# Optimization experiments

Measured on AMD Instinct MI355X. Metric: run time of the kernel, lower is better.

Reference implementation:

```python
import jax, jax.numpy as jnp
import numpy as np

N_NODES = 100000
N_EDGES = 1600000
N_GRAPHS = 256
IN_DIM, HID, OUT_DIM = 20, 128, 30954


def setup_inputs() -> dict:
    key = jax.random.key(0)
    ks = jax.random.split(key, 9)
    x = jax.random.normal(ks[0], (N_NODES, IN_DIM), dtype=jnp.float32)
    edge_index = jax.random.randint(ks[1], (2, N_EDGES), 0, N_NODES, dtype=jnp.int64)
    batch = jnp.sort(jax.random.randint(ks[2], (N_NODES,), 0, N_GRAPHS, dtype=jnp.int64))
    s = 0.05
    W1 = jax.random.normal(ks[3], (IN_DIM, HID), dtype=jnp.float32) * s
    b1 = jax.random.normal(ks[4], (HID,), dtype=jnp.float32) * s
    W2 = jax.random.normal(ks[5], (HID, HID), dtype=jnp.float32) * s
    b2 = jax.random.normal(ks[6], (HID,), dtype=jnp.float32) * s
    Wc = jax.random.normal(ks[7], (HID, OUT_DIM), dtype=jnp.float32) * s
    bc = jax.random.normal(ks[8], (OUT_DIM,), dtype=jnp.float32) * s
    return {"x": x, "edge_index": edge_index, "batch": batch,
            "W1": W1, "b1": b1, "W2": W2, "b2": b2, "Wc": Wc, "bc": bc}


def _gcn_norm(edge_index, n_nodes):
    # add self loops (PyG GCNConv default), symmetric normalization
    loops = jnp.arange(n_nodes, dtype=edge_index.dtype)
    src = jnp.concatenate([edge_index[0], loops])
    dst = jnp.concatenate([edge_index[1], loops])
    deg = jax.ops.segment_sum(jnp.ones_like(dst, dtype=jnp.float32), dst,
                              num_segments=n_nodes)
    dinv = jnp.where(deg > 0, jax.lax.rsqrt(deg), 0.0)
    norm = dinv[src] * dinv[dst]  # [E+N]
    return src, dst, norm


def _gcn_conv(x, src, dst, norm, W, b, n_nodes):
    h = x @ W                              # [N, out] transform first (fewer msg flops)
    msg = h[src] * norm[:, None]           # gather + scale
    out = jax.ops.segment_sum(msg, dst, num_segments=n_nodes)
    return out + b


def reference(x, edge_index, batch, W1, b1, W2, b2, Wc, bc):
    n = x.shape[0]
    src, dst, norm = _gcn_norm(edge_index, n)
    h = jax.nn.relu(_gcn_conv(x, src, dst, norm, W1, b1, n))
    # dropout is identity in eval mode
    h = jax.nn.relu(_gcn_conv(h, src, dst, norm, W2, b2, n))
    # global mean pool per graph
    sums = jax.ops.segment_sum(h, batch, num_segments=N_GRAPHS)       # [G, HID]
    cnts = jax.ops.segment_sum(jnp.ones((n,), jnp.float32), batch,
                               num_segments=N_GRAPHS)
    pooled = sums / jnp.maximum(cnts, 1.0)[:, None]
    return pooled @ Wc + bc  # [G, OUT_DIM]
```

## Files before the change

### kernel.cpp

```cpp
#include <hip/hip_runtime.h>

#define HID 128
#define SCAN_B 256

__device__ __forceinline__ float bf_lo(unsigned int u) { return __uint_as_float(u << 16); }
__device__ __forceinline__ float bf_hi(unsigned int u) { return __uint_as_float(u & 0xFFFF0000u); }
__device__ __forceinline__ unsigned short f2bf(float f) {
    unsigned int u = __float_as_uint(f);
    unsigned int r = (u + 0x7FFFu + ((u >> 16) & 1u)) >> 16;
    return (unsigned short)r;
}

__global__ void detect_kernel(const unsigned int* __restrict__ p, int* __restrict__ flag) {
    if (threadIdx.x == 0 && blockIdx.x == 0) {
        int is64 = 1;
        for (int i = 0; i < 64; ++i) {
            if (p[2 * i + 1] != 0u) { is64 = 0; break; }
        }
        *flag = is64;
    }
}

__global__ void cvtdeg_kernel(const void* __restrict__ p, int* __restrict__ out,
                              int* __restrict__ deg, int E, const int* __restrict__ flag) {
    int i = blockIdx.x * blockDim.x + threadIdx.x;
    if (i < 2 * E) {
        int v = (*flag) ? (int)((const long long*)p)[i] : ((const int*)p)[i];
        out[i] = v;
        if (i >= E) atomicAdd(&deg[v], 1);
    }
}

__global__ void zero_kernel(float4* __restrict__ p, long long n4) {
    long long i = (long long)blockIdx.x * blockDim.x + threadIdx.x;
    long long stride = (long long)gridDim.x * blockDim.x;
    for (; i < n4; i += stride) p[i] = make_float4(0.f, 0.f, 0.f, 0.f);
}

__global__ void cvtx_kernel(const float* __restrict__ x, unsigned short* __restrict__ xb, int n) {
    int i = blockIdx.x * blockDim.x + threadIdx.x;
    if (i < n) xb[i] = f2bf(x[i]);
}

__global__ __launch_bounds__(SCAN_B) void scan1_kernel(const int* __restrict__ deg,
                                                       int* __restrict__ incl,
                                                       int* __restrict__ blockSums, int N) {
    __shared__ int s[SCAN_B];
    int i = blockIdx.x * SCAN_B + threadIdx.x;
    int v = (i < N) ? deg[i] : 0;
    s[threadIdx.x] = v;
    __syncthreads();
#pragma unroll
    for (int off = 1; off < SCAN_B; off <<= 1) {
        int t = (threadIdx.x >= off) ? s[threadIdx.x - off] : 0;
        __syncthreads();
        s[threadIdx.x] += t;
        __syncthreads();
    }
    if (i < N) incl[i] = s[threadIdx.x];
    if (threadIdx.x == SCAN_B - 1) blockSums[blockIdx.x] = s[SCAN_B - 1];
}

__global__ __launch_bounds__(1024) void scan2_kernel(int* __restrict__ blockSums, int nb) {
    __shared__ int s[1024];
    int v = (threadIdx.x < nb) ? blockSums[threadIdx.x] : 0;
    s[threadIdx.x] = v;
    __syncthreads();
#pragma unroll
    for (int off = 1; off < 1024; off <<= 1) {
        int t = (threadIdx.x >= off) ? s[threadIdx.x - off] : 0;
        __syncthreads();
        s[threadIdx.x] += t;
        __syncthreads();
    }
    if (threadIdx.x < nb) blockSums[threadIdx.x] = (threadIdx.x > 0) ? s[threadIdx.x - 1] : 0;
}

__global__ void scan3_kernel(const int* __restrict__ incl, const int* __restrict__ deg,
                             const int* __restrict__ blockSums, int* __restrict__ rowstart,
                             float* __restrict__ dinv, int* __restrict__ cursor,
                             int N, int E) {
    int i = blockIdx.x * blockDim.x + threadIdx.x;
    if (i < N) {
        int d = deg[i];
        rowstart[i] = incl[i] - d + blockSums[i / SCAN_B];
        dinv[i] = rsqrtf((float)(d + 1));
        cursor[i] = 0;
    }
    if (i == 0) rowstart[N] = E;
}

__global__ void scatter_kernel(const int* __restrict__ src, const int* __restrict__ dst,
                               const int* __restrict__ rowstart, int* __restrict__ cursor,
                               int2* __restrict__ elist, const float* __restrict__ dinv, int E) {
    int e = blockIdx.x * blockDim.x + threadIdx.x;
    if (e >= E) return;
    int s = src[e], d = dst[e];
    int pos = rowstart[d] + atomicAdd(&cursor[d], 1);
    float nm = dinv[s] * dinv[d];
    elist[pos] = make_int2(s, __float_as_int(nm));
}

__global__ void gstart_kernel(const void* __restrict__ bt, const int* __restrict__ flag,
                              int* __restrict__ gstart, int N, int G) {
    int g = blockIdx.x * blockDim.x + threadIdx.x;
    if (g > G) return;
    int is64 = *flag;
    int lo = 0, hi = N;
    while (lo < hi) {
        int mid = (lo + hi) >> 1;
        int v = is64 ? (int)((const long long*)bt)[mid] : ((const int*)bt)[mid];
        if (v < g) lo = mid + 1; else hi = mid;
    }
    gstart[g] = lo;
}

__global__ __launch_bounds__(256) void agg_lin1_kernel(const float* __restrict__ x,
                                                       const unsigned int* __restrict__ xb32,
                                                       const float* __restrict__ W,
                                                       const float* __restrict__ b,
                                                       unsigned int* __restrict__ h1b,
                                                       const int* __restrict__ rowstart,
                                                       const int2* __restrict__ elist,
                                                       const float* __restrict__ dinv,
                                                       int N, int IN) {
    __shared__ float Ws[20 * HID];
    __shared__ float zs[8][20];
    const int tid = threadIdx.x;
    for (int i = tid; i < IN * HID; i += 256) Ws[i] = W[i];

    const int g      = tid >> 5;
    const int lane32 = tid & 31;
    const int slot   = lane32 >> 4;
    const int l      = lane32 & 15;
    const int node   = blockIdx.x * 8 + g;
    const int half   = IN >> 1;
    const bool act   = (node < N) && (l < half);

    float accx = 0.f, accy = 0.f;
    if (node < N) {
        int beg = rowstart[node], end = rowstart[node + 1];
        int e = beg + slot;
        for (; e + 6 < end; e += 8) {
            int2 p0 = elist[e];
            int2 p1 = elist[e + 2];
            int2 p2 = elist[e + 4];
            int2 p3 = elist[e + 6];
            unsigned int u0 = act ? xb32[(size_t)p0.x * half + l] : 0u;
            unsigned int u1 = act ? xb32[(size_t)p1.x * half + l] : 0u;
            unsigned int u2 = act ? xb32[(size_t)p2.x * half + l] : 0u;
            unsigned int u3 = act ? xb32[(size_t)p3.x * half + l] : 0u;
            float n0 = __int_as_float(p0.y), n1 = __int_as_float(p1.y);
            float n2 = __int_as_float(p2.y), n3 = __int_as_float(p3.y);
            accx += bf_lo(u0) * n0 + bf_lo(u1) * n1 + bf_lo(u2) * n2 + bf_lo(u3) * n3;
            accy += bf_hi(u0) * n0 + bf_hi(u1) * n1 + bf_hi(u2) * n2 + bf_hi(u3) * n3;
        }
        for (; e < end; e += 2) {
            int2 p0 = elist[e];
            unsigned int u0 = act ? xb32[(size_t)p0.x * half + l] : 0u;
            float n0 = __int_as_float(p0.y);
            accx += bf_lo(u0) * n0;
            accy += bf_hi(u0) * n0;
        }
    }
    accx += __shfl_xor(accx, 16, 64);
    accy += __shfl_xor(accy, 16, 64);
    if (node < N && slot == 0 && l < half) {
        float di = dinv[node];
        float dd = di * di;
        zs[g][2 * l]     = accx + x[(size_t)node * IN + 2 * l] * dd;
        zs[g][2 * l + 1] = accy + x[(size_t)node * IN + 2 * l + 1] * dd;
    }
    __syncthreads();

    if (node < N) {
        const int j = lane32;
        float4 acc4 = ((const float4*)b)[j];
        for (int k = 0; k < IN; ++k) {
            float zv = zs[g][k];
            float4 w = *(const float4*)&Ws[k * HID + j * 4];
            acc4.x += zv * w.x; acc4.y += zv * w.y;
            acc4.z += zv * w.z; acc4.w += zv * w.w;
        }
        acc4.x = fmaxf(acc4.x, 0.f); acc4.y = fmaxf(acc4.y, 0.f);
        acc4.z = fmaxf(acc4.z, 0.f); acc4.w = fmaxf(acc4.w, 0.f);
        uint2 st;
        st.x = (unsigned)f2bf(acc4.x) | ((unsigned)f2bf(acc4.y) << 16);
        st.y = (unsigned)f2bf(acc4.z) | ((unsigned)f2bf(acc4.w) << 16);
        ((uint2*)h1b)[(size_t)node * 32 + j] = st;
    }
}

#define TBM 64
#define TBN 64
#define TBK 32
#define XLD (TBM + 4)

__global__ __launch_bounds__(256) void gemm128_kernel(const unsigned int* __restrict__ Ab,
                                                      const float* __restrict__ W,
                                                      unsigned short* __restrict__ Cb, int N) {
    __shared__ float xs[TBK][XLD];
    __shared__ float wsh[TBK][TBN + 4];
    const int tid = threadIdx.x;
    const int n0 = blockIdx.x * TBM;
    const int c0 = blockIdx.y * TBN;
    const int ng = tid >> 4;
    const int cg = tid & 15;
    const int anode = tid >> 2;
    const int af    = tid & 3;
    const int wk    = tid >> 4;
    const int wc    = tid & 15;

    const uint4* Av = (const uint4*)Ab;

    float acc[4][4] = {};

    for (int k0 = 0; k0 < HID; k0 += TBK) {
        {
            int gn = n0 + anode;
            uint4 u = make_uint4(0u, 0u, 0u, 0u);
            if (gn < N) u = Av[(size_t)gn * 16 + (k0 >> 3) + af];
            int kb = af * 8;
            xs[kb + 0][anode] = bf_lo(u.x);
            xs[kb + 1][anode] = bf_hi(u.x);
            xs[kb + 2][anode] = bf_lo(u.y);
            xs[kb + 3][anode] = bf_hi(u.y);
            xs[kb + 4][anode] = bf_lo(u.z);
            xs[kb + 5][anode] = bf_hi(u.z);
            xs[kb + 6][anode] = bf_lo(u.w);
            xs[kb + 7][anode] = bf_hi(u.w);
        }
#pragma unroll
        for (int r = 0; r < 2; ++r) {
            int kk = wk + r * 16;
            *(float4*)&wsh[kk][wc * 4] =
                *(const float4*)(W + (size_t)(k0 + kk) * HID + c0 + wc * 4);
        }
        __syncthreads();
#pragma unroll
        for (int kk = 0; kk < TBK; ++kk) {
            float a[4], b[4];
            *(float4*)a = *(const float4*)&xs[kk][ng * 4];
            *(float4*)b = *(const float4*)&wsh[kk][cg * 4];
#pragma unroll
            for (int m = 0; m < 4; ++m)
#pragma unroll
                for (int n = 0; n < 4; ++n) acc[m][n] += a[m] * b[n];
        }
        __syncthreads();
    }

#pragma unroll
    for (int m = 0; m < 4; ++m) {
        int gn = n0 + ng * 4 + m;
        if (gn < N) {
            ushort4 st;
            st.x = f2bf(acc[m][0]); st.y = f2bf(acc[m][1]);
            st.z = f2bf(acc[m][2]); st.w = f2bf(acc[m][3]);
            *(ushort4*)(Cb + (size_t)gn * HID + c0 + cg * 4) = st;
        }
    }
}

__global__ __launch_bounds__(256) void csr_aggb_kernel(const unsigned short* __restrict__ h2b,
                                                       unsigned short* __restrict__ outb,
                                                       const int* __restrict__ rowstart,
                                                       const int2* __restrict__ elist,
                                                       const float* __restrict__ dinv,
                                                       const float* __restrict__ bias,
                                                       int N) {
    int node = blockIdx.x * 16 + (threadIdx.x >> 4);
    if (node >= N) return;
    int q = threadIdx.x & 15;
    const uint4* hv = (const uint4*)h2b;
    float acc[8] = {};
    int beg = rowstart[node], end = rowstart[node + 1];
    int e = beg;
    for (; e + 3 < end; e += 4) {
        int2 p0 = elist[e];
        int2 p1 = elist[e + 1];
        int2 p2 = elist[e + 2];
        int2 p3 = elist[e + 3];
        uint4 a0 = hv[(size_t)p0.x * 16 + q];
        uint4 a1 = hv[(size_t)p1.x * 16 + q];
        uint4 a2 = hv[(size_t)p2.x * 16 + q];
        uint4 a3 = hv[(size_t)p3.x * 16 + q];
        float n0 = __int_as_float(p0.y), n1 = __int_as_float(p1.y);
        float n2 = __int_as_float(p2.y), n3 = __int_as_float(p3.y);
        acc[0] += bf_lo(a0.x) * n0 + bf_lo(a1.x) * n1 + bf_lo(a2.x) * n2 + bf_lo(a3.x) * n3;
        acc[1] += bf_hi(a0.x) * n0 + bf_hi(a1.x) * n1 + bf_hi(a2.x) * n2 + bf_hi(a3.x) * n3;
        acc[2] += bf_lo(a0.y) * n0 + bf_lo(a1.y) * n1 + bf_lo(a2.y) * n2 + bf_lo(a3.y) * n3;
        acc[3] += bf_hi(a0.y) * n0 + bf_hi(a1.y) * n1 + bf_hi(a2.y) * n2 + bf_hi(a3.y) * n3;
        acc[4] += bf_lo(a0.z) * n0 + bf_lo(a1.z) * n1 + bf_lo(a2.z) * n2 + bf_lo(a3.z) * n3;
        acc[5] += bf_hi(a0.z) * n0 + bf_hi(a1.z) * n1 + bf_hi(a2.z) * n2 + bf_hi(a3.z) * n3;
        acc[6] += bf_lo(a0.w) * n0 + bf_lo(a1.w) * n1 + bf_lo(a2.w) * n2 + bf_lo(a3.w) * n3;
        acc[7] += bf_hi(a0.w) * n0 + bf_hi(a1.w) * n1 + bf_hi(a2.w) * n2 + bf_hi(a3.w) * n3;
    }
    for (; e < end; ++e) {
        int2 p0 = elist[e];
        uint4 a0 = hv[(size_t)p0.x * 16 + q];
        float n0 = __int_as_float(p0.y);
        acc[0] += bf_lo(a0.x) * n0; acc[1] += bf_hi(a0.x) * n0;
        acc[2] += bf_lo(a0.y) * n0; acc[3] += bf_hi(a0.y) * n0;
        acc[4] += bf_lo(a0.z) * n0; acc[5] += bf_hi(a0.z) * n0;
        acc[6] += bf_lo(a0.w) * n0; acc[7] += bf_hi(a0.w) * n0;
    }
    float di = dinv[node];
    float dd = di * di;
    uint4 sv = hv[(size_t)node * 16 + q];
    float self[8] = { bf_lo(sv.x), bf_hi(sv.x), bf_lo(sv.y), bf_hi(sv.y),
                      bf_lo(sv.z), bf_hi(sv.z), bf_lo(sv.w), bf_hi(sv.w) };
    float4 b0 = ((const float4*)bias)[2 * q];
    float4 b1 = ((const float4*)bias)[2 * q + 1];
    float r[8];
    r[0] = fmaxf(acc[0] + self[0] * dd + b0.x, 0.f);
    r[1] = fmaxf(acc[1] + self[1] * dd + b0.y, 0.f);
    r[2] = fmaxf(acc[2] + self[2] * dd + b0.z, 0.f);
    r[3] = fmaxf(acc[3] + self[3] * dd + b0.w, 0.f);
    r[4] = fmaxf(acc[4] + self[4] * dd + b1.x, 0.f);
    r[5] = fmaxf(acc[5] + self[5] * dd + b1.y, 0.f);
    r[6] = fmaxf(acc[6] + self[6] * dd + b1.z, 0.f);
    r[7] = fmaxf(acc[7] + self[7] * dd + b1.w, 0.f);
    uint4 st;
    st.x = (unsigned)f2bf(r[0]) | ((unsigned)f2bf(r[1]) << 16);
    st.y = (unsigned)f2bf(r[2]) | ((unsigned)f2bf(r[3]) << 16);
    st.z = (unsigned)f2bf(r[4]) | ((unsigned)f2bf(r[5]) << 16);
    st.w = (unsigned)f2bf(r[6]) | ((unsigned)f2bf(r[7]) << 16);
    ((uint4*)outb)[(size_t)node * 16 + q] = st;
}

__global__ __launch_bounds__(1024) void pool2_kernel(const unsigned short* __restrict__ hb,
                                                     const int* __restrict__ gstart,
                                                     float* __restrict__ meanp, int G) {
    int g = blockIdx.x;
    int part = threadIdx.x >> 7;
    int j = threadIdx.x & 127;
    int beg = gstart[g], end = gstart[g + 1];
    float s = 0.f;
    for (int n = beg + part; n < end; n += 8)
        s += __uint_as_float(((unsigned)hb[(size_t)n * HID + j]) << 16);
    __shared__ float red[8][HID];
    red[part][j] = s;
    __syncthreads();
    if (part == 0) {
        float tot = 0.f;
#pragma unroll
        for (int r = 0; r < 8; ++r) tot += red[r][j];
        float c = (float)(end - beg);
        meanp[(size_t)g * HID + j] = tot / fmaxf(c, 1.f);
    }
}

#define CBM 64
#define CBN 64
#define CBK 32

__global__ __launch_bounds__(256) void clsgemm_kernel(const float* __restrict__ A,
                                                      const float* __restrict__ Bw,
                                                      const float* __restrict__ bc,
                                                      float* __restrict__ C,
                                                      int G, int OUT) {
    __shared__ float as[CBK][CBM + 4];
    __shared__ float bs[CBK][CBN + 4];
    const int tid = threadIdx.x;
    const int g0 = blockIdx.y * CBM;
    const int c0 = blockIdx.x * CBN;
    const int mg = tid >> 4;
    const int cg = tid & 15;
    const int arow = tid >> 3;
    const int af   = tid & 7;
    const int wk   = tid >> 4;
    const int wc   = tid & 15;

    float acc[4][4] = {};

    for (int k0 = 0; k0 < HID; k0 += CBK) {
#pragma unroll
        for (int r = 0; r < 2; ++r) {
            int row = arow + r * 32;
            int g = g0 + row;
            float4 v = make_float4(0.f, 0.f, 0.f, 0.f);
            if (g < G) v = *(const float4*)(A + (size_t)g * HID + k0 + af * 4);
            as[af * 4 + 0][row] = v.x;
            as[af * 4 + 1][row] = v.y;
            as[af * 4 + 2][row] = v.z;
            as[af * 4 + 3][row] = v.w;
        }
#pragma unroll
        for (int r = 0; r < 2; ++r) {
            int kk = wk + r * 16;
            int c = c0 + wc * 4;
            const float* bp = Bw + (size_t)(k0 + kk) * OUT + c;
            float2 lo = make_float2(0.f, 0.f), hi = make_float2(0.f, 0.f);
            if (c + 3 < OUT) {
                lo = *(const float2*)bp;
                hi = *(const float2*)(bp + 2);
            } else {
                if (c + 0 < OUT) lo.x = bp[0];
                if (c + 1 < OUT) lo.y = bp[1];
                if (c + 2 < OUT) hi.x = bp[2];
                if (c + 3 < OUT) hi.y = bp[3];
            }
            bs[kk][wc * 4 + 0] = lo.x;
            bs[kk][wc * 4 + 1] = lo.y;
            bs[kk][wc * 4 + 2] = hi.x;
            bs[kk][wc * 4 + 3] = hi.y;
        }
        __syncthreads();
#pragma unroll
        for (int kk = 0; kk < CBK; ++kk) {
            float a[4], b[4];
            *(float4*)a = *(const float4*)&as[kk][mg * 4];
            *(float4*)b = *(const float4*)&bs[kk][cg * 4];
#pragma unroll
            for (int m = 0; m < 4; ++m)
#pragma unroll
                for (int n = 0; n < 4; ++n) acc[m][n] += a[m] * b[n];
        }
        __syncthreads();
    }

    int c = c0 + cg * 4;
    float b0 = (c + 0 < OUT) ? bc[c + 0] : 0.f;
    float b1 = (c + 1 < OUT) ? bc[c + 1] : 0.f;
    float b2 = (c + 2 < OUT) ? bc[c + 2] : 0.f;
    float b3 = (c + 3 < OUT) ? bc[c + 3] : 0.f;
#pragma unroll
    for (int m = 0; m < 4; ++m) {
        int g = g0 + mg * 4 + m;
        if (g >= G) continue;
        float* cp = C + (size_t)g * OUT + c;
        if (c + 3 < OUT) {
            *(float2*)cp = make_float2(acc[m][0] + b0, acc[m][1] + b1);
            *(float2*)(cp + 2) = make_float2(acc[m][2] + b2, acc[m][3] + b3);
        } else {
            if (c + 0 < OUT) cp[0] = acc[m][0] + b0;
            if (c + 1 < OUT) cp[1] = acc[m][1] + b1;
            if (c + 2 < OUT) cp[2] = acc[m][2] + b2;
            if (c + 3 < OUT) cp[3] = acc[m][3] + b3;
        }
    }
}

extern "C" void kernel_launch(void* const* d_in, const int* in_sizes, int n_in,
                              void* d_out, int out_size, void* d_ws, size_t ws_size,
                              hipStream_t stream) {
    const float* x  = (const float*)d_in[0];
    const void*  ei = d_in[1];
    const void*  bt = d_in[2];
    const float* W1 = (const float*)d_in[3];
    const float* b1 = (const float*)d_in[4];
    const float* W2 = (const float*)d_in[5];
    const float* b2 = (const float*)d_in[6];
    const float* Wc = (const float*)d_in[7];
    const float* bc = (const float*)d_in[8];
    float* out = (float*)d_out;

    const int N   = in_sizes[2];
    const int E   = in_sizes[1] / 2;
    const int IN  = in_sizes[0] / N;
    const int OUT = in_sizes[8];
    const int G   = out_size / OUT;

    char* ws = (char*)d_ws;
    size_t off = 0;
    auto alloc = [&](size_t bytes) {
        size_t p = off;
        off += (bytes + 255) & ~(size_t)255;
        return p;
    };
    int*            idx32    = (int*)(ws + alloc((size_t)2 * E * 4));
    int*            deg      = (int*)(ws + alloc((size_t)N * 4));
    float*          dinv     = (float*)(ws + alloc((size_t)N * 4));
    int*            incl     = (int*)(ws + alloc((size_t)N * 4));
    int*            rowstart = (int*)(ws + alloc((size_t)(N + 1) * 4));
    int*            cursor   = (int*)(ws + alloc((size_t)N * 4));
    int*            blockSums= (int*)(ws + alloc((size_t)1024 * 4));
    int2*           elist    = (int2*)(ws + alloc((size_t)E * 8));
    unsigned short* xb       = (unsigned short*)(ws + alloc((size_t)N * IN * 2));
    unsigned int*   h1b      = (unsigned int*)(ws + alloc((size_t)N * HID * 2));
    unsigned short* h2b      = (unsigned short*)(ws + alloc((size_t)N * HID * 2));
    unsigned short* houtb    = (unsigned short*)(ws + alloc((size_t)N * HID * 2));
    int*            gstart   = (int*)(ws + alloc((size_t)(G + 1) * 4));
    float*          meanp    = (float*)(ws + alloc((size_t)G * HID * 4));
    int*            flag     = (int*)(ws + alloc(4));
    (void)ws_size;

    int* srcI = idx32;
    int* dstI = idx32 + E;

    const int B = 256;
    const int nb = (N + SCAN_B - 1) / SCAN_B;

    detect_kernel<<<1, 64, 0, stream>>>((const unsigned int*)ei, flag);
    zero_kernel<<<256, B, 0, stream>>>((float4*)deg, (long long)N / 4);
    cvtdeg_kernel<<<(2 * E + B - 1) / B, B, 0, stream>>>(ei, idx32, deg, E, flag);
    cvtx_kernel<<<(N * IN + B - 1) / B, B, 0, stream>>>(x, xb, N * IN);

    scan1_kernel<<<nb, SCAN_B, 0, stream>>>(deg, incl, blockSums, N);
    scan2_kernel<<<1, 1024, 0, stream>>>(blockSums, nb);
    scan3_kernel<<<(N + B - 1) / B, B, 0, stream>>>(incl, deg, blockSums, rowstart,
                                                    dinv, cursor, N, E);
    scatter_kernel<<<(E + B - 1) / B, B, 0, stream>>>(srcI, dstI, rowstart, cursor, elist, dinv, E);

    gstart_kernel<<<2, 256, 0, stream>>>(bt, flag, gstart, N, G);

    agg_lin1_kernel<<<(N + 7) / 8, 256, 0, stream>>>(x, (const unsigned int*)xb, W1, b1,
                                                     h1b, rowstart, elist, dinv, N, IN);

    {
        dim3 grid((N + TBM - 1) / TBM, HID / TBN);
        gemm128_kernel<<<grid, 256, 0, stream>>>(h1b, W2, h2b, N);
    }
    csr_aggb_kernel<<<(N + 15) / 16, 256, 0, stream>>>(h2b, houtb, rowstart, elist, dinv, b2, N);

    pool2_kernel<<<G, 1024, 0, stream>>>(houtb, gstart, meanp, G);

    {
        dim3 grid((OUT + CBN - 1) / CBN, (G + CBM - 1) / CBM);
        clsgemm_kernel<<<grid, 256, 0, stream>>>(meanp, Wc, bc, out, G, OUT);
    }
}
```

Measured before the change: 376.8 us.

## Build CSR via two-pass bucketed scatter with shared-memory cursors; fuse small kernels

Replaces the single-pass CSR scatter, which used per-node global atomics and fully random writes, with a two-level approach. Edges are first binned into buckets of 128 destination nodes using per-bucket global atomic counters. A second kernel then places each edge within its bucket using shared-memory cursors, so the final elist writes stay local. Separately, the zero and detect kernels are merged and gstart is folded into scan3 to cut launch count. The cost is an extra staging buffer and an extra pass over E edges, plus heavy atomic contention on the roughly 782 bucket counters.

```diff
diff --git a/kernel.cpp b/kernel.cpp
--- a/kernel.cpp
+++ b/kernel.cpp
@@ -2,6 +2,8 @@
 
 #define HID 128
 #define SCAN_B 256
+#define BUCK_SHIFT 7
+#define BUCK_SIZE 128
 
 __device__ __forceinline__ float bf_lo(unsigned int u) { return __uint_as_float(u << 16); }
 __device__ __forceinline__ float bf_hi(unsigned int u) { return __uint_as_float(u & 0xFFFF0000u); }
@@ -11,14 +13,18 @@
     return (unsigned short)r;
 }
 
-__global__ void detect_kernel(const unsigned int* __restrict__ p, int* __restrict__ flag) {
-    if (threadIdx.x == 0 && blockIdx.x == 0) {
+__global__ void init_kernel(const unsigned int* __restrict__ p, int* __restrict__ flag,
+                            float4* __restrict__ deg4, long long n4) {
+    if (blockIdx.x == 0 && threadIdx.x == 0) {
         int is64 = 1;
         for (int i = 0; i < 64; ++i) {
             if (p[2 * i + 1] != 0u) { is64 = 0; break; }
         }
         *flag = is64;
     }
+    long long i = (long long)blockIdx.x * blockDim.x + threadIdx.x;
+    long long stride = (long long)gridDim.x * blockDim.x;
+    for (; i < n4; i += stride) deg4[i] = make_float4(0.f, 0.f, 0.f, 0.f);
 }
 
 __global__ void cvtdeg_kernel(const void* __restrict__ p, int* __restrict__ out,
@@ -29,12 +35,6 @@
         out[i] = v;
         if (i >= E) atomicAdd(&deg[v], 1);
     }
-}
-
-__global__ void zero_kernel(float4* __restrict__ p, long long n4) {
-    long long i = (long long)blockIdx.x * blockDim.x + threadIdx.x;
-    long long stride = (long long)gridDim.x * blockDim.x;
-    for (; i < n4; i += stride) p[i] = make_float4(0.f, 0.f, 0.f, 0.f);
 }
 
 __global__ void cvtx_kernel(const float* __restrict__ x, unsigned short* __restrict__ xb, int n) {
@@ -79,6 +79,8 @@
 __global__ void scan3_kernel(const int* __restrict__ incl, const int* __restrict__ deg,
                              const int* __restrict__ blockSums, int* __restrict__ rowstart,
                              float* __restrict__ dinv, int* __restrict__ cursor,
+                             const void* __restrict__ bt, const int* __restrict__ flag,
+                             int* __restrict__ gstart, int G,
                              int N, int E) {
     int i = blockIdx.x * blockDim.x + threadIdx.x;
     if (i < N) {
@@ -88,31 +90,53 @@
         cursor[i] = 0;
     }
     if (i == 0) rowstart[N] = E;
-}
-
-__global__ void scatter_kernel(const int* __restrict__ src, const int* __restrict__ dst,
-                               const int* __restrict__ rowstart, int* __restrict__ cursor,
-                               int2* __restrict__ elist, const float* __restrict__ dinv, int E) {
+    if (i <= G) {
+        int is64 = *flag;
+        int lo = 0, hi = N;
+        while (lo < hi) {
+            int mid = (lo + hi) >> 1;
+            int v = is64 ? (int)((const long long*)bt)[mid] : ((const int*)bt)[mid];
+            if (v < i) lo = mid + 1; else hi = mid;
+        }
+        gstart[i] = lo;
+    }
+}
+
+__global__ void bucketA_kernel(const int* __restrict__ src, const int* __restrict__ dst,
+                               const int* __restrict__ rowstart, int* __restrict__ bcursor,
+                               int2* __restrict__ staging, int E) {
     int e = blockIdx.x * blockDim.x + threadIdx.x;
     if (e >= E) return;
     int s = src[e], d = dst[e];
-    int pos = rowstart[d] + atomicAdd(&cursor[d], 1);
-    float nm = dinv[s] * dinv[d];
-    elist[pos] = make_int2(s, __float_as_int(nm));
-}
-
-__global__ void gstart_kernel(const void* __restrict__ bt, const int* __restrict__ flag,
-                              int* __restrict__ gstart, int N, int G) {
-    int g = blockIdx.x * blockDim.x + threadIdx.x;
-    if (g > G) return;
-    int is64 = *flag;
-    int lo = 0, hi = N;
-    while (lo < hi) {
-        int mid = (lo + hi) >> 1;
-        int v = is64 ? (int)((const long long*)bt)[mid] : ((const int*)bt)[mid];
-        if (v < g) lo = mid + 1; else hi = mid;
-    }
-    gstart[g] = lo;
+    int b = d >> BUCK_SHIFT;
+    int base = rowstart[b << BUCK_SHIFT];
+    int pos = base + atomicAdd(&bcursor[b], 1);
+    staging[pos] = make_int2(s, d);
+}
+
+__global__ __launch_bounds__(256) void bucketB_kernel(const int2* __restrict__ staging,
+                                                      const int* __restrict__ rowstart,
+                                                      const float* __restrict__ dinv,
+                                                      int2* __restrict__ elist, int N) {
+    __shared__ int cur[BUCK_SIZE];
+    __shared__ float dl[BUCK_SIZE];
+    int n0 = blockIdx.x << BUCK_SHIFT;
+    int n1 = min(N, n0 + BUCK_SIZE);
+    int cnt = n1 - n0;
+    if (threadIdx.x < cnt) {
+        cur[threadIdx.x] = rowstart[n0 + threadIdx.x];
+        dl[threadIdx.x] = dinv[n0 + threadIdx.x];
+    }
+    __syncthreads();
+    int base = rowstart[n0];
+    int limit = rowstart[n1];
+    for (int i = base + threadIdx.x; i < limit; i += 256) {
+        int2 sd = staging[i];
+        int loc = sd.y - n0;
+        int pos = atomicAdd(&cur[loc], 1);
+        float nm = dinv[sd.x] * dl[loc];
+        elist[pos] = make_int2(sd.x, __float_as_int(nm));
+    }
 }
 
 __global__ __launch_bounds__(256) void agg_lin1_kernel(const float* __restrict__ x,
@@ -477,6 +501,7 @@
     int*            cursor   = (int*)(ws + alloc((size_t)N * 4));
     int*            blockSums= (int*)(ws + alloc((size_t)1024 * 4));
     int2*           elist    = (int2*)(ws + alloc((size_t)E * 8));
+    int2*           staging  = (int2*)(ws + alloc((size_t)E * 8));
     unsigned short* xb       = (unsigned short*)(ws + alloc((size_t)N * IN * 2));
     unsigned int*   h1b      = (unsigned int*)(ws + alloc((size_t)N * HID * 2));
     unsigned short* h2b      = (unsigned short*)(ws + alloc((size_t)N * HID * 2));
@@ -491,19 +516,20 @@
 
     const int B = 256;
     const int nb = (N + SCAN_B - 1) / SCAN_B;
-
-    detect_kernel<<<1, 64, 0, stream>>>((const unsigned int*)ei, flag);
-    zero_kernel<<<256, B, 0, stream>>>((float4*)deg, (long long)N / 4);
+    const int nbuck = (N + BUCK_SIZE - 1) / BUCK_SIZE;
+
+    init_kernel<<<256, B, 0, stream>>>((const unsigned int*)ei, flag, (float4*)deg,
+                                       (long long)N / 4);
     cvtdeg_kernel<<<(2 * E + B - 1) / B, B, 0, stream>>>(ei, idx32, deg, E, flag);
     cvtx_kernel<<<(N * IN + B - 1) / B, B, 0, stream>>>(x, xb, N * IN);
 
     scan1_kernel<<<nb, SCAN_B, 0, stream>>>(deg, incl, blockSums, N);
     scan2_kernel<<<1, 1024, 0, stream>>>(blockSums, nb);
     scan3_kernel<<<(N + B - 1) / B, B, 0, stream>>>(incl, deg, blockSums, rowstart,
-                                                    dinv, cursor, N, E);
-    scatter_kernel<<<(E + B - 1) / B, B, 0, stream>>>(srcI, dstI, rowstart, cursor, elist, dinv, E);
-
-    gstart_kernel<<<2, 256, 0, stream>>>(bt, flag, gstart, N, G);
+                                                    dinv, cursor, bt, flag, gstart, G, N, E);
+    bucketA_kernel<<<(E + B - 1) / B, B, 0, stream>>>(srcI, dstI, rowstart, cursor,
+                                                      staging, E);
+    bucketB_kernel<<<nbuck, 256, 0, stream>>>(staging, rowstart, dinv, elist, N);
 
     agg_lin1_kernel<<<(N + 7) / 8, 256, 0, stream>>>(x, (const unsigned int*)xb, W1, b1,
                                                      h1b, rowstart, elist, dinv, N, IN);
```

Measured after the change: 700.6 us. 1.86x slower.
